# Performance work log

Hardware: AMD Instinct MI355X
Metric: run time of the kernel (lower is better)

Reference implementation:

```python
import jax, jax.numpy as jnp
from jax import lax
import numpy as np

B, H, W, C = 64, 64, 64, 8          # batch, grid, channel_n (C=8 is structurally required)
PC = 3 * C                           # perceive output channels = 24
FIRE_RATE = 0.5
ALPHA_THR = 0.1

def _conv(x, w, b, padding):
    y = lax.conv_general_dilated(x, w, (1, 1), padding,
                                 dimension_numbers=('NHWC', 'HWIO', 'NHWC'))
    return y + b

def _dwconv(x, k):
    # k: [kh, kw, Cin, mult] (TF depthwise layout) -> grouped conv rhs [kh, kw, 1, Cin*mult]
    kh, kw, cin, m = k.shape
    rhs = k.reshape(kh, kw, 1, cin * m)
    return lax.conv_general_dilated(x, rhs, (1, 1), 'SAME',
                                    dimension_numbers=('NHWC', 'HWIO', 'NHWC'),
                                    feature_group_count=cin)

def _maxpool3(a):
    return lax.reduce_window(a, -jnp.inf, lax.max, (1, 3, 3, 1), (1, 1, 1, 1), 'SAME')

def setup_inputs() -> dict:
    key = jax.random.key(0)
    ks = jax.random.split(key, 12)
    d_flat = H * W * PC                       # 98304
    d_att = 3 * 3 * 24 * 3                    # 648
    s = lambda *sh: 0.02
    return {
        'x': jax.random.normal(ks[0], (B, H, W, C), jnp.float32),
        'update_noise': jax.random.uniform(ks[1], (B, H, W, 1), jnp.float32),
        'W_att': jax.random.normal(ks[2], (d_flat, d_att), jnp.float32) * 0.002,
        'b_att': jax.random.normal(ks[3], (d_att,), jnp.float32) * 0.02,
        'W1': jax.random.normal(ks[4], (3, 3, 3 * PC, 48), jnp.float32) * 0.05,
        'b1': jax.random.normal(ks[5], (48,), jnp.float32) * 0.02,
        'Wt': jax.random.normal(ks[6], (3, 3, 48, 48), jnp.float32) * 0.05,
        'bt': jax.random.normal(ks[7], (48,), jnp.float32) * 0.02,
        'W2': jax.random.normal(ks[8], (1, 1, 48, 128), jnp.float32) * 0.05,
        'b2': jax.random.normal(ks[9], (128,), jnp.float32) * 0.02,
        'W3': jax.random.normal(ks[10], (1, 1, 128, C), jnp.float32) * 0.05,
        'b3': jax.random.normal(ks[11], (C,), jnp.float32) * 0.02,
    }

def reference(x, update_noise, W_att, b_att, W1, b1, Wt, bt, W2, b2, W3, b3):
    # --- fixed perceive stencil (angle = 0) ---
    ident = np.outer(np.float32([0, 1, 0]), np.float32([0, 1, 0]))
    dxk = np.outer(np.float32([1, 0, 1]), np.float32([1, 0, 1])) / 8.0
    dyk = dxk.T
    k = jnp.stack([jnp.asarray(ident), jnp.asarray(dxk), jnp.asarray(dyk)], -1)  # [3,3,3]
    k = jnp.tile(k[:, :, None, :], (1, 1, C, 1))                                 # [3,3,C,3]

    pre_life = _maxpool3(x[:, :, :, 3:4]) > ALPHA_THR

    y = _dwconv(x, k)                                     # [B,H,W,24]
    # global attention: flatten -> dense -> reshape, take sample 0's kernel
    y_sum = (y.reshape(y.shape[0], -1) @ W_att + b_att).reshape(-1, 3, 3, 24, 3)[0]
    y = _dwconv(y, y_sum)                                 # [B,H,W,72]
    y = y * lax.rsqrt(jnp.maximum(jnp.sum(y * y), 1e-12))  # global l2_normalize

    # dmodel: conv3 VALID -> convT3 VALID -> 1x1 relu -> 1x1
    h = _conv(y, W1, b1, 'VALID')                         # [B,62,62,48]
    h = lax.conv_transpose(h, Wt, (1, 1), 'VALID',
                           dimension_numbers=('NHWC', 'HWIO', 'NHWC')) + bt  # [B,64,64,48]
    h = jax.nn.relu(_conv(h, W2, b2, 'SAME'))             # [B,64,64,128]
    dx_out = _conv(h, W3, b3, 'SAME')                     # [B,64,64,C], step_size = 1.0

    update_mask = (update_noise <= FIRE_RATE).astype(x.dtype)
    x2 = x + dx_out * update_mask

    post_life = _maxpool3(x2[:, :, :, 3:4]) > ALPHA_THR
    life = jnp.logical_and(pre_life, post_life).astype(x.dtype)
    return x2 * life
```

## Files before the change

kernel.cpp:

```cpp
#include <hip/hip_runtime.h>

#define NB 64
#define HW 4096

__global__ __launch_bounds__(256) void k_perceive(
    const float* __restrict__ x, float* __restrict__ y_chw,
    float* __restrict__ y0_hwc, float* __restrict__ prelife,
    float* __restrict__ att_zero, const float* __restrict__ W2,
    float* __restrict__ W2T) {
  int t = threadIdx.x;
  if (blockIdx.x == 1024) {
    for (int i = t; i < 6144; i += 256) {
      int o = i / 48;
      int c = i - o * 48;
      W2T[i] = W2[c * 128 + o];
    }
    return;
  }
  if (blockIdx.x == 0) {
    for (int i = t; i < 649; i += 256) att_zero[i] = 0.f;
  }
  int pix = blockIdx.x * 256 + t;
  int b = pix >> 12;
  int hw = pix & 4095;
  int h = hw >> 6, w = hw & 63;
  const float* xp = x + (size_t)pix * 8;
  bool hm = h > 0, hp = h < 63, wm = w > 0, wp = w < 63;

  float mx = -1e30f;
  #pragma unroll
  for (int di = -1; di <= 1; ++di) {
    if ((unsigned)(h + di) > 63u) continue;
    #pragma unroll
    for (int dj = -1; dj <= 1; ++dj) {
      if ((unsigned)(w + dj) > 63u) continue;
      mx = fmaxf(mx, xp[(di * 64 + dj) * 8 + 3]);
    }
  }
  prelife[pix] = (mx > 0.1f) ? 1.f : 0.f;

  float* yb = y_chw + (size_t)b * 16 * HW + hw;
  bool b0 = (b == 0);
  #pragma unroll
  for (int c = 0; c < 8; ++c) {
    float ctr = xp[c];
    float a00 = (hm && wm) ? xp[(-65) * 8 + c] : 0.f;
    float a02 = (hm && wp) ? xp[(-63) * 8 + c] : 0.f;
    float a20 = (hp && wm) ? xp[(63) * 8 + c] : 0.f;
    float a22 = (hp && wp) ? xp[(65) * 8 + c] : 0.f;
    float d = (a00 + a02 + a20 + a22) * 0.125f;
    yb[(size_t)(c * 2 + 0) * HW] = ctr;
    yb[(size_t)(c * 2 + 1) * HW] = d;
    if (b0) {
      float* y0p = y0_hwc + hw * 24 + c * 3;
      y0p[0] = ctr; y0p[1] = d; y0p[2] = d;
    }
  }
}

__global__ __launch_bounds__(256) void k_att(
    const float* __restrict__ y0, const float* __restrict__ Watt,
    float* __restrict__ att_acc) {
  int t = threadIdx.x;
  int r0 = blockIdx.x * 128;
  float a0 = 0.f, a1 = 0.f, a2 = 0.f;
  for (int r = 0; r < 128; ++r) {
    float yv = y0[r0 + r];
    const float* wr = Watt + (size_t)(r0 + r) * 648;
    a0 = fmaf(yv, wr[t], a0);
    a1 = fmaf(yv, wr[t + 256], a1);
    if (t < 136) a2 = fmaf(yv, wr[t + 512], a2);
  }
  atomicAdd(att_acc + t, a0);
  atomicAdd(att_acc + t + 256, a1);
  if (t < 136) atomicAdd(att_acc + t + 512, a2);
}

__global__ __launch_bounds__(256) void k_ssqfold(
    const float* __restrict__ y_chw, const float* __restrict__ att_acc,
    const float* __restrict__ b_att, float* __restrict__ ssq,
    const float* __restrict__ W1, float* __restrict__ K16) {
  __shared__ float ys[648];
  __shared__ float s[16 * 324];
  int t = threadIdx.x;

  if (blockIdx.x >= 1024) {
    for (int i = t; i < 648; i += 256) ys[i] = att_acc[i] + b_att[i];
    __syncthreads();
    int r = blockIdx.x - 1024;
    int ri = r / 5, rj = r - ri * 5;
    #pragma unroll
    for (int k = 0; k < 3; ++k) {
      int idx = t + 256 * k;
      int p = idx / 48;
      int o = idx - p * 48;
      int c = p >> 1, tt = p & 1;
      float acc = 0.f;
      for (int ki = 0; ki < 3; ++ki) {
        int qi = ri - ki;
        if ((unsigned)qi > 2u) continue;
        for (int kj = 0; kj < 3; ++kj) {
          int qj = rj - kj;
          if ((unsigned)qj > 2u) continue;
          int k9 = ki * 3 + kj, q9 = qi * 3 + qj;
          const float* wb = W1 + (size_t)(k9 * 72 + 9 * c) * 48 + o;
          const float* yb = ys + q9 * 72 + 9 * c;
          if (tt == 0) {
            #pragma unroll
            for (int m = 0; m < 3; ++m) acc = fmaf(wb[(size_t)m * 48], yb[m], acc);
          } else {
            #pragma unroll
            for (int m = 0; m < 3; ++m) {
              acc = fmaf(wb[(size_t)(3 + m) * 48], yb[3 + m], acc);
              acc = fmaf(wb[(size_t)(6 + m) * 48], yb[6 + m], acc);
            }
          }
        }
      }
      K16[(size_t)(r * 16 + p) * 48 + o] = acc;
    }
    return;
  }

  for (int i = t; i < 648; i += 256) ys[i] = att_acc[i] + b_att[i];

  int blk = blockIdx.x;
  int b = blk >> 4;
  int tile = blk & 15;
  int i0 = (tile >> 2) * 16;
  int j0 = (tile & 3) * 16;
  const float* yb = y_chw + (size_t)b * 16 * HW;

  for (int idx = t; idx < 16 * 324; idx += 256) {
    int c = idx / 324;
    int pos = idx - c * 324;
    int r = pos / 18, col = pos - r * 18;
    int gr = i0 - 1 + r, gc = j0 - 1 + col;
    bool v = ((unsigned)gr < 64u) && ((unsigned)gc < 64u);
    s[idx] = v ? yb[(size_t)c * HW + gr * 64 + gc] : 0.f;
  }
  __syncthreads();

  int ty = t >> 4, tx = t & 15;
  float local = 0.f;
  for (int c = 0; c < 8; ++c) {
    float tapA[9], tapB[9];
    const float* sa = s + (size_t)(2 * c) * 324 + ty * 18 + tx;
    const float* sb = s + (size_t)(2 * c + 1) * 324 + ty * 18 + tx;
    #pragma unroll
    for (int di = 0; di < 3; ++di)
      #pragma unroll
      for (int dj = 0; dj < 3; ++dj) {
        tapA[di * 3 + dj] = sa[di * 18 + dj];
        tapB[di * 3 + dj] = sb[di * 18 + dj];
      }
    #pragma unroll
    for (int m = 0; m < 3; ++m) {
      float z0 = 0.f, z1 = 0.f, z2 = 0.f;
      #pragma unroll
      for (int k9 = 0; k9 < 9; ++k9) {
        z0 = fmaf(tapA[k9], ys[k9 * 72 + 9 * c + m], z0);
        z1 = fmaf(tapB[k9], ys[k9 * 72 + 9 * c + 3 + m], z1);
        z2 = fmaf(tapB[k9], ys[k9 * 72 + 9 * c + 6 + m], z2);
      }
      local += z0 * z0 + z1 * z1 + z2 * z2;
    }
  }
  #pragma unroll
  for (int off = 32; off; off >>= 1) local += __shfl_down(local, off, 64);
  if ((t & 63) == 0) atomicAdd(ssq, local);
}

__global__ __launch_bounds__(256, 4) void k_conv1f(
    const float* __restrict__ y_chw, const float* __restrict__ K16,
    const float* __restrict__ b1, const float* __restrict__ ssqp,
    float* __restrict__ h1) {
  __shared__ float s[8 * 400];
  int t = threadIdx.x;
  int og = __builtin_amdgcn_readfirstlane(t >> 7);
  int sub = t & 127;
  int ty = sub >> 4, tx = sub & 15;
  int blk = blockIdx.x;
  int b = blk >> 4;
  int tile = blk & 15;
  int i0 = (tile >> 2) * 16; if (i0 > 46) i0 = 46;
  int j0 = (tile & 3) * 16;  if (j0 > 46) j0 = 46;

  const float* yb = y_chw + (size_t)b * 16 * HW;
  float acc0[24], acc1[24];
  #pragma unroll
  for (int o = 0; o < 24; ++o) { acc0[o] = 0.f; acc1[o] = 0.f; }

  for (int c0 = 0; c0 < 16; c0 += 8) {
    __syncthreads();
    for (int idx = t; idx < 8 * 400; idx += 256) {
      int c = idx / 400;
      int pos = idx - c * 400;
      int r = pos / 20, col = pos - r * 20;
      int gr = i0 - 1 + r, gc = j0 - 1 + col;
      bool v = ((unsigned)gr < 64u) && ((unsigned)gc < 64u);
      s[idx] = v ? yb[(size_t)(c0 + c) * HW + gr * 64 + gc] : 0.f;
    }
    __syncthreads();
    for (int c = 0; c < 8; ++c) {
      const float* sc = s + (size_t)c * 400 + ty * 20 + tx;
      #pragma unroll
      for (int ri = 0; ri < 5; ++ri) {
        float t0[5], t1[5];
        #pragma unroll
        for (int rj = 0; rj < 5; ++rj) {
          t0[rj] = sc[ri * 20 + rj];
          t1[rj] = sc[(ri + 8) * 20 + rj];
        }
        #pragma unroll
        for (int rj = 0; rj < 5; ++rj) {
          const float* w = K16 + (size_t)((ri * 5 + rj) * 16 + c0 + c) * 48 + og * 24;
          float tv0 = t0[rj], tv1 = t1[rj];
          #pragma unroll
          for (int o = 0; o < 24; ++o) {
            acc0[o] = fmaf(tv0, w[o], acc0[o]);
            acc1[o] = fmaf(tv1, w[o], acc1[o]);
          }
        }
      }
    }
  }
  float inv = rsqrtf(fmaxf(ssqp[0], 1e-12f));
  float* hb = h1 + (size_t)b * 48 * 3844 + (size_t)og * 24 * 3844
            + (i0 + ty) * 62 + (j0 + tx);
  #pragma unroll
  for (int o = 0; o < 24; ++o) {
    float bo = b1[og * 24 + o];
    hb[(size_t)o * 3844] = fmaf(acc0[o], inv, bo);
    hb[(size_t)o * 3844 + 8 * 62] = fmaf(acc1[o], inv, bo);
  }
}

__global__ __launch_bounds__(256, 4) void k_convTh(
    const float* __restrict__ h1, const float* __restrict__ Wt,
    const float* __restrict__ bt, const float* __restrict__ W2T,
    const float* __restrict__ b2, const float* __restrict__ W3,
    const float* __restrict__ b3, const float* __restrict__ x,
    const float* __restrict__ noise, float* __restrict__ x2,
    float* __restrict__ alpha2) {
  __shared__ float s[12 * 324];
  int t = threadIdx.x;
  int og = __builtin_amdgcn_readfirstlane(t >> 7);
  int sub = t & 127;
  int ty = sub >> 4, tx = sub & 15;
  int blk = blockIdx.x;
  int b = blk >> 4;
  int tile = blk & 15;
  int i0 = (tile >> 2) * 16;
  int j0 = (tile & 3) * 16;

  float acc0[24], acc1[24];
  #pragma unroll
  for (int o = 0; o < 24; ++o) { acc0[o] = 0.f; acc1[o] = 0.f; }
  const float* hb = h1 + (size_t)b * 48 * 3844;

  for (int c0 = 0; c0 < 48; c0 += 12) {
    __syncthreads();
    for (int idx = t; idx < 12 * 324; idx += 256) {
      int c = idx / 324;
      int pos = idx - c * 324;
      int r = pos / 18, col = pos - r * 18;
      int gr = i0 - 2 + r, gc = j0 - 2 + col;
      bool v = ((unsigned)gr < 62u) && ((unsigned)gc < 62u);
      s[idx] = v ? hb[(size_t)(c0 + c) * 3844 + gr * 62 + gc] : 0.f;
    }
    __syncthreads();
    for (int c = 0; c < 12; ++c) {
      const float* sc = s + c * 324 + ty * 18 + tx;
      float tap0[9], tap1[9];
      #pragma unroll
      for (int di = 0; di < 3; ++di)
        #pragma unroll
        for (int dj = 0; dj < 3; ++dj) {
          tap0[di * 3 + dj] = sc[di * 18 + dj];
          tap1[di * 3 + dj] = sc[(di + 8) * 18 + dj];
        }
      #pragma unroll
      for (int k9 = 0; k9 < 9; ++k9) {
        const float* w = Wt + (size_t)(k9 * 48 + c0 + c) * 48 + og * 24;
        float tv0 = tap0[k9], tv1 = tap1[k9];
        #pragma unroll
        for (int o = 0; o < 24; ++o) {
          acc0[o] = fmaf(tv0, w[o], acc0[o]);
          acc1[o] = fmaf(tv1, w[o], acc1[o]);
        }
      }
    }
  }

  float hr[48];
  #pragma unroll
  for (int ph = 0; ph < 4; ++ph) {
    __syncthreads();
    if (og == (ph >> 1)) {
      #pragma unroll
      for (int o = 0; o < 12; ++o) {
        int oo = (ph & 1) * 12 + o;
        float bo = bt[ph * 12 + o];
        s[o * 256 + ty * 16 + tx] = acc0[oo] + bo;
        s[o * 256 + (ty + 8) * 16 + tx] = acc1[oo] + bo;
      }
    }
    __syncthreads();
    #pragma unroll
    for (int c = 0; c < 12; ++c) hr[ph * 12 + c] = s[c * 256 + t];
  }

  int pty = t >> 4, ptx = t & 15;
  int pix = b * 4096 + (i0 + pty) * 64 + (j0 + ptx);
  float dx[8];
  #pragma unroll
  for (int k = 0; k < 8; ++k) dx[k] = b3[k];
  #pragma unroll 4
  for (int o = 0; o < 128; ++o) {
    float v = b2[o];
    const float* w2 = W2T + o * 48;
    #pragma unroll
    for (int c = 0; c < 48; ++c) v = fmaf(hr[c], w2[c], v);
    v = fmaxf(v, 0.f);
    const float* w3 = W3 + o * 8;
    #pragma unroll
    for (int k = 0; k < 8; ++k) dx[k] = fmaf(v, w3[k], dx[k]);
  }
  float m = (noise[pix] <= 0.5f) ? 1.f : 0.f;
  const float* xp = x + (size_t)pix * 8;
  float* xo = x2 + (size_t)pix * 8;
  float a3 = 0.f;
  #pragma unroll
  for (int k = 0; k < 8; ++k) {
    float v = fmaf(dx[k], m, xp[k]);
    xo[k] = v;
    if (k == 3) a3 = v;
  }
  alpha2[pix] = a3;
}

__global__ __launch_bounds__(256) void k_life(
    const float* __restrict__ x2, const float* __restrict__ alpha2,
    const float* __restrict__ prelife, float* __restrict__ out) {
  int pix = blockIdx.x * 256 + threadIdx.x;
  int hw = pix & 4095;
  int h = hw >> 6, w = hw & 63;
  const float* ab = alpha2 + (size_t)(pix - hw);
  float mx = -1e30f;
  #pragma unroll
  for (int di = -1; di <= 1; ++di) {
    if ((unsigned)(h + di) > 63u) continue;
    #pragma unroll
    for (int dj = -1; dj <= 1; ++dj) {
      if ((unsigned)(w + dj) > 63u) continue;
      mx = fmaxf(mx, ab[(h + di) * 64 + (w + dj)]);
    }
  }
  float life = (mx > 0.1f && prelife[pix] > 0.5f) ? 1.f : 0.f;
  const float* xp = x2 + (size_t)pix * 8;
  float* op = out + (size_t)pix * 8;
  #pragma unroll
  for (int k = 0; k < 8; ++k) op[k] = xp[k] * life;
}

extern "C" void kernel_launch(void* const* d_in, const int* in_sizes, int n_in,
                              void* d_out, int out_size, void* d_ws, size_t ws_size,
                              hipStream_t stream) {
  const float* x     = (const float*)d_in[0];
  const float* noise = (const float*)d_in[1];
  const float* Watt  = (const float*)d_in[2];
  const float* b_att = (const float*)d_in[3];
  const float* W1    = (const float*)d_in[4];
  const float* b1    = (const float*)d_in[5];
  const float* Wt    = (const float*)d_in[6];
  const float* bt    = (const float*)d_in[7];
  const float* W2    = (const float*)d_in[8];
  const float* b2    = (const float*)d_in[9];
  const float* W3    = (const float*)d_in[10];
  const float* b3    = (const float*)d_in[11];
  float* out = (float*)d_out;

  float* ws = (float*)d_ws;
  size_t o_y   = 0;
  size_t o_h1  = o_y + 4194304;
  size_t o_y0  = o_h1 + 11808768;
  size_t o_pre = o_y0 + 98304;
  size_t o_att = o_pre + 262144;
  size_t o_w2t = o_att + 652;
  size_t o_k16 = o_w2t + 6144;
  float* y_chw   = ws + o_y;
  float* h1_chw  = ws + o_h1;
  float* y0_hwc  = ws + o_y0;
  float* prelife = ws + o_pre;
  float* att_acc = ws + o_att;
  float* ssq     = ws + o_att + 648;
  float* W2T     = ws + o_w2t;
  float* K16     = ws + o_k16;
  float* x2      = ws + o_y;
  float* alpha2  = ws + o_y + 2097152;

  k_perceive<<<1025, 256, 0, stream>>>(x, y_chw, y0_hwc, prelife, att_acc, W2, W2T);
  k_att<<<768, 256, 0, stream>>>(y0_hwc, Watt, att_acc);
  k_ssqfold<<<1049, 256, 0, stream>>>(y_chw, att_acc, b_att, ssq, W1, K16);
  k_conv1f<<<1024, 256, 0, stream>>>(y_chw, K16, b1, ssq, h1_chw);
  k_convTh<<<1024, 256, 0, stream>>>(h1_chw, Wt, bt, W2T, b2, W3, b3, x, noise, x2, alpha2);
  k_life<<<1024, 256, 0, stream>>>(x2, alpha2, prelife, out);
}
```

Baseline: 853.1 us.

## Halve per-thread tiles in conv kernels and split 1x1 MLP across thread groups

Both conv1f and convTh now have each thread compute one output pixel instead of two. Tiles become 8x16 and the grid doubles to 2048 blocks, with higher launch-bound occupancy targets (8 and 6). In convTh, the two 128-thread halves each compute 64 of the 128 hidden units of the 1x1 MLP and combine their partial dx sums through shared memory, rather than each thread doing all 128. The aim is lower register pressure and more waves in flight, at the cost of more halo reloads per output, less weight reuse per load, and extra barriers.

```diff
diff --git a/kernel.cpp b/kernel.cpp
--- a/kernel.cpp
+++ b/kernel.cpp
@@ -171,31 +171,31 @@
   if ((t & 63) == 0) atomicAdd(ssq, local);
 }
 
-__global__ __launch_bounds__(256, 4) void k_conv1f(
+__global__ __launch_bounds__(256, 8) void k_conv1f(
     const float* __restrict__ y_chw, const float* __restrict__ K16,
     const float* __restrict__ b1, const float* __restrict__ ssqp,
     float* __restrict__ h1) {
-  __shared__ float s[8 * 400];
+  __shared__ float s[8 * 240];
   int t = threadIdx.x;
   int og = __builtin_amdgcn_readfirstlane(t >> 7);
   int sub = t & 127;
   int ty = sub >> 4, tx = sub & 15;
   int blk = blockIdx.x;
-  int b = blk >> 4;
-  int tile = blk & 15;
-  int i0 = (tile >> 2) * 16; if (i0 > 46) i0 = 46;
+  int b = blk >> 5;
+  int tile = blk & 31;
+  int i0 = (tile >> 2) * 8;  if (i0 > 54) i0 = 54;
   int j0 = (tile & 3) * 16;  if (j0 > 46) j0 = 46;
 
   const float* yb = y_chw + (size_t)b * 16 * HW;
-  float acc0[24], acc1[24];
-  #pragma unroll
-  for (int o = 0; o < 24; ++o) { acc0[o] = 0.f; acc1[o] = 0.f; }
+  float acc[24];
+  #pragma unroll
+  for (int o = 0; o < 24; ++o) acc[o] = 0.f;
 
   for (int c0 = 0; c0 < 16; c0 += 8) {
     __syncthreads();
-    for (int idx = t; idx < 8 * 400; idx += 256) {
-      int c = idx / 400;
-      int pos = idx - c * 400;
+    for (int idx = t; idx < 8 * 240; idx += 256) {
+      int c = idx / 240;
+      int pos = idx - c * 240;
       int r = pos / 20, col = pos - r * 20;
       int gr = i0 - 1 + r, gc = j0 - 1 + col;
       bool v = ((unsigned)gr < 64u) && ((unsigned)gc < 64u);
@@ -203,24 +203,18 @@
     }
     __syncthreads();
     for (int c = 0; c < 8; ++c) {
-      const float* sc = s + (size_t)c * 400 + ty * 20 + tx;
+      const float* sc = s + c * 240 + ty * 20 + tx;
       #pragma unroll
       for (int ri = 0; ri < 5; ++ri) {
-        float t0[5], t1[5];
+        float t0[5];
         #pragma unroll
-        for (int rj = 0; rj < 5; ++rj) {
-          t0[rj] = sc[ri * 20 + rj];
-          t1[rj] = sc[(ri + 8) * 20 + rj];
-        }
+        for (int rj = 0; rj < 5; ++rj) t0[rj] = sc[ri * 20 + rj];
         #pragma unroll
         for (int rj = 0; rj < 5; ++rj) {
           const float* w = K16 + (size_t)((ri * 5 + rj) * 16 + c0 + c) * 48 + og * 24;
-          float tv0 = t0[rj], tv1 = t1[rj];
+          float tv = t0[rj];
           #pragma unroll
-          for (int o = 0; o < 24; ++o) {
-            acc0[o] = fmaf(tv0, w[o], acc0[o]);
-            acc1[o] = fmaf(tv1, w[o], acc1[o]);
-          }
+          for (int o = 0; o < 24; ++o) acc[o] = fmaf(tv, w[o], acc[o]);
         }
       }
     }
@@ -229,95 +223,86 @@
   float* hb = h1 + (size_t)b * 48 * 3844 + (size_t)og * 24 * 3844
             + (i0 + ty) * 62 + (j0 + tx);
   #pragma unroll
-  for (int o = 0; o < 24; ++o) {
-    float bo = b1[og * 24 + o];
-    hb[(size_t)o * 3844] = fmaf(acc0[o], inv, bo);
-    hb[(size_t)o * 3844 + 8 * 62] = fmaf(acc1[o], inv, bo);
-  }
-}
-
-__global__ __launch_bounds__(256, 4) void k_convTh(
+  for (int o = 0; o < 24; ++o)
+    hb[(size_t)o * 3844] = fmaf(acc[o], inv, b1[og * 24 + o]);
+}
+
+__global__ __launch_bounds__(256, 6) void k_convTh(
     const float* __restrict__ h1, const float* __restrict__ Wt,
     const float* __restrict__ bt, const float* __restrict__ W2T,
     const float* __restrict__ b2, const float* __restrict__ W3,
     const float* __restrict__ b3, const float* __restrict__ x,
     const float* __restrict__ noise, float* __restrict__ x2,
     float* __restrict__ alpha2) {
-  __shared__ float s[12 * 324];
+  __shared__ float s[24 * 180];
   int t = threadIdx.x;
   int og = __builtin_amdgcn_readfirstlane(t >> 7);
   int sub = t & 127;
   int ty = sub >> 4, tx = sub & 15;
   int blk = blockIdx.x;
-  int b = blk >> 4;
-  int tile = blk & 15;
-  int i0 = (tile >> 2) * 16;
+  int b = blk >> 5;
+  int tile = blk & 31;
+  int i0 = (tile >> 2) * 8;
   int j0 = (tile & 3) * 16;
 
-  float acc0[24], acc1[24];
-  #pragma unroll
-  for (int o = 0; o < 24; ++o) { acc0[o] = 0.f; acc1[o] = 0.f; }
+  float acc[24];
+  #pragma unroll
+  for (int o = 0; o < 24; ++o) acc[o] = 0.f;
   const float* hb = h1 + (size_t)b * 48 * 3844;
 
-  for (int c0 = 0; c0 < 48; c0 += 12) {
+  for (int c0 = 0; c0 < 48; c0 += 24) {
     __syncthreads();
-    for (int idx = t; idx < 12 * 324; idx += 256) {
-      int c = idx / 324;
-      int pos = idx - c * 324;
+    for (int idx = t; idx < 24 * 180; idx += 256) {
+      int c = idx / 180;
+      int pos = idx - c * 180;
       int r = pos / 18, col = pos - r * 18;
       int gr = i0 - 2 + r, gc = j0 - 2 + col;
       bool v = ((unsigned)gr < 62u) && ((unsigned)gc < 62u);
       s[idx] = v ? hb[(size_t)(c0 + c) * 3844 + gr * 62 + gc] : 0.f;
     }
     __syncthreads();
-    for (int c = 0; c < 12; ++c) {
-      const float* sc = s + c * 324 + ty * 18 + tx;
-      float tap0[9], tap1[9];
+    for (int c = 0; c < 24; ++c) {
+      const float* sc = s + c * 180 + ty * 18 + tx;
+      float tap[9];
       #pragma unroll
       for (int di = 0; di < 3; ++di)
         #pragma unroll
-        for (int dj = 0; dj < 3; ++dj) {
-          tap0[di * 3 + dj] = sc[di * 18 + dj];
-          tap1[di * 3 + dj] = sc[(di + 8) * 18 + dj];
-        }
+        for (int dj = 0; dj < 3; ++dj) tap[di * 3 + dj] = sc[di * 18 + dj];
       #pragma unroll
       for (int k9 = 0; k9 < 9; ++k9) {
         const float* w = Wt + (size_t)(k9 * 48 + c0 + c) * 48 + og * 24;
-        float tv0 = tap0[k9], tv1 = tap1[k9];
+        float tv = tap[k9];
         #pragma unroll
-        for (int o = 0; o < 24; ++o) {
-          acc0[o] = fmaf(tv0, w[o], acc0[o]);
-          acc1[o] = fmaf(tv1, w[o], acc1[o]);
-        }
+        for (int o = 0; o < 24; ++o) acc[o] = fmaf(tv, w[o], acc[o]);
       }
     }
   }
 
   float hr[48];
-  #pragma unroll
-  for (int ph = 0; ph < 4; ++ph) {
-    __syncthreads();
-    if (og == (ph >> 1)) {
-      #pragma unroll
-      for (int o = 0; o < 12; ++o) {
-        int oo = (ph & 1) * 12 + o;
-        float bo = bt[ph * 12 + o];
-        s[o * 256 + ty * 16 + tx] = acc0[oo] + bo;
-        s[o * 256 + (ty + 8) * 16 + tx] = acc1[oo] + bo;
-      }
-    }
-    __syncthreads();
-    #pragma unroll
-    for (int c = 0; c < 12; ++c) hr[ph * 12 + c] = s[c * 256 + t];
-  }
-
-  int pty = t >> 4, ptx = t & 15;
-  int pix = b * 4096 + (i0 + pty) * 64 + (j0 + ptx);
+  __syncthreads();
+  if (og == 0) {
+    #pragma unroll
+    for (int o = 0; o < 24; ++o) s[o * 128 + sub] = acc[o] + bt[o];
+  }
+  __syncthreads();
+  #pragma unroll
+  for (int c = 0; c < 24; ++c) hr[c] = s[c * 128 + sub];
+  __syncthreads();
+  if (og == 1) {
+    #pragma unroll
+    for (int o = 0; o < 24; ++o) s[o * 128 + sub] = acc[o] + bt[24 + o];
+  }
+  __syncthreads();
+  #pragma unroll
+  for (int c = 0; c < 24; ++c) hr[24 + c] = s[c * 128 + sub];
+
+  int pix = b * 4096 + (i0 + ty) * 64 + (j0 + tx);
   float dx[8];
   #pragma unroll
-  for (int k = 0; k < 8; ++k) dx[k] = b3[k];
+  for (int k = 0; k < 8; ++k) dx[k] = og ? 0.f : b3[k];
   #pragma unroll 4
-  for (int o = 0; o < 128; ++o) {
+  for (int oo = 0; oo < 64; ++oo) {
+    int o = og * 64 + oo;
     float v = b2[o];
     const float* w2 = W2T + o * 48;
     #pragma unroll
@@ -327,17 +312,27 @@
     #pragma unroll
     for (int k = 0; k < 8; ++k) dx[k] = fmaf(v, w3[k], dx[k]);
   }
-  float m = (noise[pix] <= 0.5f) ? 1.f : 0.f;
-  const float* xp = x + (size_t)pix * 8;
-  float* xo = x2 + (size_t)pix * 8;
-  float a3 = 0.f;
-  #pragma unroll
-  for (int k = 0; k < 8; ++k) {
-    float v = fmaf(dx[k], m, xp[k]);
-    xo[k] = v;
-    if (k == 3) a3 = v;
-  }
-  alpha2[pix] = a3;
+  __syncthreads();
+  if (og == 1) {
+    #pragma unroll
+    for (int k = 0; k < 8; ++k) s[sub * 9 + k] = dx[k];
+  }
+  __syncthreads();
+  if (og == 0) {
+    #pragma unroll
+    for (int k = 0; k < 8; ++k) dx[k] += s[sub * 9 + k];
+    float m = (noise[pix] <= 0.5f) ? 1.f : 0.f;
+    const float* xp = x + (size_t)pix * 8;
+    float* xo = x2 + (size_t)pix * 8;
+    float a3 = 0.f;
+    #pragma unroll
+    for (int k = 0; k < 8; ++k) {
+      float v = fmaf(dx[k], m, xp[k]);
+      xo[k] = v;
+      if (k == 3) a3 = v;
+    }
+    alpha2[pix] = a3;
+  }
 }
 
 __global__ __launch_bounds__(256) void k_life(
@@ -403,7 +398,7 @@
   k_perceive<<<1025, 256, 0, stream>>>(x, y_chw, y0_hwc, prelife, att_acc, W2, W2T);
   k_att<<<768, 256, 0, stream>>>(y0_hwc, Watt, att_acc);
   k_ssqfold<<<1049, 256, 0, stream>>>(y_chw, att_acc, b_att, ssq, W1, K16);
-  k_conv1f<<<1024, 256, 0, stream>>>(y_chw, K16, b1, ssq, h1_chw);
-  k_convTh<<<1024, 256, 0, stream>>>(h1_chw, Wt, bt, W2T, b2, W3, b3, x, noise, x2, alpha2);
+  k_conv1f<<<2048, 256, 0, stream>>>(y_chw, K16, b1, ssq, h1_chw);
+  k_convTh<<<2048, 256, 0, stream>>>(h1_chw, Wt, bt, W2T, b2, W3, b3, x, noise, x2, alpha2);
   k_life<<<1024, 256, 0, stream>>>(x2, alpha2, prelife, out);
 }
```

Result: slower. 880.5 us (+3.2%).
